# Optimization experiments

Measured on AMD Instinct MI355X. Metric: run time of the kernel, lower is better.

Reference implementation:

```python
import jax
jax.config.update("jax_enable_x64", True)
import jax.numpy as jnp
import numpy as np

LEAF_VOXEL_SIZE = 0.1
SCALE_UP_FACTOR = 2.0
VOXEL_LEVEL_NUM = 4
BUFFER_SIZE = 4194304
FEATURE_DIM = 8
N_FEATURES = 500000
N_QUERY = 1000000
FEATURE_STD = 0.01

PRIMES = jnp.array([73856093, 19349669, 83492791], dtype=jnp.int64)
# 8 voxel-corner offsets, matching self.steps ordering (z fastest)
STEPS = jnp.array([[0,0,0],[0,0,1],[0,1,0],[0,1,1],[1,0,0],[1,0,1],[1,1,0],[1,1,1]], dtype=jnp.float32)


def setup_inputs() -> dict:
    key = jax.random.key(0)
    k1, k2, k3, k4 = jax.random.split(key, 4)
    # query points spread over a few meters of scene
    query_points = 5.0 * jax.random.normal(k1, (N_QUERY, 3), dtype=jnp.float32)
    features = FEATURE_STD * jax.random.normal(k2, (VOXEL_LEVEL_NUM, N_FEATURES, FEATURE_DIM), dtype=jnp.float32)
    idx = jax.random.randint(k3, (VOXEL_LEVEL_NUM, BUFFER_SIZE), 0, N_FEATURES, dtype=jnp.int64)
    empty = jax.random.uniform(k4, (VOXEL_LEVEL_NUM, BUFFER_SIZE)) < 0.05
    feature_indexs = jnp.where(empty, jnp.int64(-1), idx)
    return {"query_points": query_points, "features": features, "feature_indexs": feature_indexs}


def _interp_coeffs(q, vs):
    # trilinear weights in the same corner order as STEPS -> [N, 8]
    d = q / vs - jnp.floor(q / vs)           # [N,3]
    tx, ty, tz = d[:, 0], d[:, 1], d[:, 2]
    w = jnp.stack([
        (1-tx)*(1-ty)*(1-tz), (1-tx)*(1-ty)*tz, (1-tx)*ty*(1-tz), (1-tx)*ty*tz,
        tx*(1-ty)*(1-tz),     tx*(1-ty)*tz,     tx*ty*(1-tz),     tx*ty*tz,
    ], axis=-1)
    return w


def reference(query_points, features, feature_indexs):
    N = query_points.shape[0]
    sum_features = jnp.zeros((N, FEATURE_DIM), dtype=jnp.float32)
    valid_mask = jnp.ones((N,), dtype=bool)
    for i in range(VOXEL_LEVEL_NUM):
        vs = LEAF_VOXEL_SIZE * SCALE_UP_FACTOR ** i
        grids = jnp.floor(query_points / vs)                       # [N,3]
        corners = (grids[:, None, :] + STEPS).astype(jnp.int64)    # [N,8,3]
        keys = (corners * PRIMES).sum(-1) % BUFFER_SIZE            # [N,8]
        idx = feature_indexs[i][keys]                              # [N,8]
        mask = idx.min(axis=1) >= 0                                # [N]
        safe_idx = jnp.maximum(idx, 0)
        feats = features[i][safe_idx]                              # [N,8,D]
        coeffs = _interp_coeffs(query_points, vs)                  # [N,8]
        contrib = jnp.einsum('ncd,nc->nd', feats, coeffs)          # [N,D]
        sum_features = sum_features + jnp.where(mask[:, None], contrib, 0.0)
        if i == 0:
            valid_mask = mask
    return sum_features, valid_mask
```

## Files before the change

### kernel.cpp

```cpp
#include <hip/hip_runtime.h>

#define BUF_MASK 4194303u
#define BUF_SIZE 4194304
#define NFEAT 500000
#define FDIM 8
#define NLVL 4
#define NBINS 262144
#define NXCD 8

typedef float f4 __attribute__((ext_vector_type(4)));

__global__ void detect_int64_kernel(const unsigned int* __restrict__ fi,
                                    int* __restrict__ flag) {
    if (blockIdx.x == 0 && threadIdx.x == 0) {
        int cnt = 0;
        for (int k = 0; k < 128; ++k) {
            unsigned int w = fi[2 * k + 1];
            cnt += (w == 0u || w == 0xFFFFFFFFu) ? 1 : 0;
        }
        *flag = (cnt >= 96) ? 1 : 0;
    }
}

__device__ __forceinline__ unsigned part3(unsigned x) {
    x &= 0x3FFu;
    x = (x | (x << 16)) & 0x030000FFu;
    x = (x | (x << 8))  & 0x0300F00Fu;
    x = (x | (x << 4))  & 0x030C30C3u;
    x = (x | (x << 2))  & 0x09249249u;
    return x;
}

__global__ __launch_bounds__(256) void bin_kernel(
    const float* __restrict__ qp, unsigned* __restrict__ hist,
    unsigned* __restrict__ binA, unsigned* __restrict__ rankA, int N)
{
    int i = blockIdx.x * blockDim.x + threadIdx.x;
    if (i >= N) return;
    float x = qp[3 * (size_t)i + 0];
    float y = qp[3 * (size_t)i + 1];
    float z = qp[3 * (size_t)i + 2];
    int cx = (int)floorf(x * 1.25f) + 32;
    int cy = (int)floorf(y * 1.25f) + 32;
    int cz = (int)floorf(z * 1.25f) + 32;
    cx = min(max(cx, 0), 63); cy = min(max(cy, 0), 63); cz = min(max(cz, 0), 63);
    unsigned m = (part3((unsigned)cx) << 2) | (part3((unsigned)cy) << 1) | part3((unsigned)cz);
    unsigned r = atomicAdd(&hist[m], 1u);
    binA[i] = m; rankA[i] = r;
}

__global__ __launch_bounds__(512) void scan_block(
    const unsigned* __restrict__ hist, unsigned* __restrict__ starts,
    unsigned* __restrict__ bsum)
{
    __shared__ unsigned tmp[512];
    int b = blockIdx.x, t = threadIdx.x;
    unsigned v = hist[(size_t)b * 512 + t];
    tmp[t] = v; __syncthreads();
    for (int o = 1; o < 512; o <<= 1) {
        unsigned add = (t >= o) ? tmp[t - o] : 0u;
        __syncthreads();
        tmp[t] += add;
        __syncthreads();
    }
    starts[(size_t)b * 512 + t] = tmp[t] - v;
    if (t == 511) bsum[b] = tmp[t];
}

__global__ __launch_bounds__(512) void scan_sums(unsigned* __restrict__ bsum) {
    __shared__ unsigned tmp[512];
    int t = threadIdx.x;
    unsigned v = bsum[t];
    tmp[t] = v; __syncthreads();
    for (int o = 1; o < 512; o <<= 1) {
        unsigned add = (t >= o) ? tmp[t - o] : 0u;
        __syncthreads();
        tmp[t] += add;
        __syncthreads();
    }
    bsum[t] = tmp[t] - v;
}

__global__ __launch_bounds__(512) void scan_add(
    unsigned* __restrict__ starts, const unsigned* __restrict__ bsum)
{
    starts[(size_t)blockIdx.x * 512 + threadIdx.x] += bsum[blockIdx.x];
}

__global__ __launch_bounds__(256) void scatter_kernel(
    const float* __restrict__ qp, const unsigned* __restrict__ binA,
    const unsigned* __restrict__ rankA, const unsigned* __restrict__ starts,
    float4* __restrict__ sorted, int N)
{
    int i = blockIdx.x * blockDim.x + threadIdx.x;
    if (i >= N) return;
    unsigned pos = starts[binA[i]] + rankA[i];
    sorted[pos] = make_float4(qp[3 * (size_t)i + 0], qp[3 * (size_t)i + 1],
                              qp[3 * (size_t)i + 2], __uint_as_float((unsigned)i));
}

__global__ __launch_bounds__(256) void nvh_sorted_kernel(
    const f4* __restrict__ sq,
    const float* __restrict__ feats,
    const int*   __restrict__ fidx,
    const int*   __restrict__ flagp,
    float* __restrict__ out,
    int N)
{
    unsigned nwg = gridDim.x, b = blockIdx.x;
    unsigned q = nwg / NXCD, r = nwg % NXCD;
    unsigned xcd = b % NXCD, off = b / NXCD;
    unsigned swz = (xcd < r ? xcd * (q + 1) : r * (q + 1) + (xcd - r) * q) + off;
    int i = (int)(swz * blockDim.x + threadIdx.x);
    if (i >= N) return;
    const int shift = *flagp;

    f4 qv = sq[i];
    float qx = qv.x, qy = qv.y, qz = qv.z;
    unsigned orig = __float_as_uint(qv.w);

    float frx[NLVL], fry[NLVL], frz[NLVL];
    int   idxs[NLVL][8];

    #pragma unroll
    for (int l = 0; l < NLVL; ++l) {
        const float vs = 0.1f * (float)(1 << l);
        float tx = qx / vs, ty = qy / vs, tz = qz / vs;
        float gx = floorf(tx), gy = floorf(ty), gz = floorf(tz);
        frx[l] = tx - gx; fry[l] = ty - gy; frz[l] = tz - gz;
        unsigned h = (unsigned)(int)gx * 73856093u
                   + (unsigned)(int)gy * 19349669u
                   + (unsigned)(int)gz * 83492791u;
        const int* base = fidx + (((size_t)l * BUF_SIZE) << shift);
        #pragma unroll
        for (int c = 0; c < 8; ++c) {
            unsigned key = h;
            if (c & 4) key += 73856093u;
            if (c & 2) key += 19349669u;
            if (c & 1) key += 83492791u;
            key &= BUF_MASK;
            idxs[l][c] = base[(size_t)key << shift];
        }
    }

    float acc[8] = {0.f, 0.f, 0.f, 0.f, 0.f, 0.f, 0.f, 0.f};
    float maskv = 0.0f;

    #pragma unroll
    for (int l = 0; l < NLVL; ++l) {
        int mn = idxs[l][0];
        #pragma unroll
        for (int c = 1; c < 8; ++c) mn = min(mn, idxs[l][c]);
        float m = (mn >= 0) ? 1.0f : 0.0f;
        if (l == 0) maskv = m;
        const float* fb = feats + (size_t)l * (size_t)NFEAT * FDIM;
        float tx = frx[l], ty = fry[l], tz = frz[l];
        float sx[2] = {1.0f - tx, tx};
        float sy[2] = {1.0f - ty, ty};
        float sz[2] = {1.0f - tz, tz};
        #pragma unroll
        for (int c = 0; c < 8; ++c) {
            float w = m * ((sx[(c >> 2) & 1] * sy[(c >> 1) & 1]) * sz[c & 1]);
            const f4* f4p = (const f4*)(fb + (size_t)max(idxs[l][c], 0) * FDIM);
            f4 a = f4p[0];
            f4 b2 = f4p[1];
            acc[0] += w * a.x;  acc[1] += w * a.y;
            acc[2] += w * a.z;  acc[3] += w * a.w;
            acc[4] += w * b2.x; acc[5] += w * b2.y;
            acc[6] += w * b2.z; acc[7] += w * b2.w;
        }
    }

    f4 o0 = {acc[0], acc[1], acc[2], acc[3]};
    f4 o1 = {acc[4], acc[5], acc[6], acc[7]};
    f4* op = (f4*)(out + (size_t)orig * 8);
    op[0] = o0;
    op[1] = o1;
    out[(size_t)8 * N + orig] = maskv;
}

__global__ __launch_bounds__(256) void nvh_kernel(
    const float* __restrict__ qp, const float* __restrict__ feats,
    const int* __restrict__ fidx, const int* __restrict__ flagp,
    float* __restrict__ out, int N)
{
    int i = blockIdx.x * blockDim.x + threadIdx.x;
    if (i >= N) return;
    const int shift = *flagp;
    float qx = qp[3 * (size_t)i + 0];
    float qy = qp[3 * (size_t)i + 1];
    float qz = qp[3 * (size_t)i + 2];
    float frx[NLVL], fry[NLVL], frz[NLVL];
    int   idxs[NLVL][8];
    #pragma unroll
    for (int l = 0; l < NLVL; ++l) {
        const float vs = 0.1f * (float)(1 << l);
        float tx = qx / vs, ty = qy / vs, tz = qz / vs;
        float gx = floorf(tx), gy = floorf(ty), gz = floorf(tz);
        frx[l] = tx - gx; fry[l] = ty - gy; frz[l] = tz - gz;
        unsigned h = (unsigned)(int)gx * 73856093u
                   + (unsigned)(int)gy * 19349669u
                   + (unsigned)(int)gz * 83492791u;
        const int* base = fidx + (((size_t)l * BUF_SIZE) << shift);
        #pragma unroll
        for (int c = 0; c < 8; ++c) {
            unsigned key = h;
            if (c & 4) key += 73856093u;
            if (c & 2) key += 19349669u;
            if (c & 1) key += 83492791u;
            key &= BUF_MASK;
            idxs[l][c] = base[(size_t)key << shift];
        }
    }
    float acc[8] = {0.f, 0.f, 0.f, 0.f, 0.f, 0.f, 0.f, 0.f};
    float maskv = 0.0f;
    #pragma unroll
    for (int l = 0; l < NLVL; ++l) {
        int mn = idxs[l][0];
        #pragma unroll
        for (int c = 1; c < 8; ++c) mn = min(mn, idxs[l][c]);
        float m = (mn >= 0) ? 1.0f : 0.0f;
        if (l == 0) maskv = m;
        const float* fb = feats + (size_t)l * (size_t)NFEAT * FDIM;
        float tx = frx[l], ty = fry[l], tz = frz[l];
        float sx[2] = {1.0f - tx, tx};
        float sy[2] = {1.0f - ty, ty};
        float sz[2] = {1.0f - tz, tz};
        #pragma unroll
        for (int c = 0; c < 8; ++c) {
            float w = m * ((sx[(c >> 2) & 1] * sy[(c >> 1) & 1]) * sz[c & 1]);
            const f4* f4p = (const f4*)(fb + (size_t)max(idxs[l][c], 0) * FDIM);
            f4 a = f4p[0];
            f4 b2 = f4p[1];
            acc[0] += w * a.x;  acc[1] += w * a.y;
            acc[2] += w * a.z;  acc[3] += w * a.w;
            acc[4] += w * b2.x; acc[5] += w * b2.y;
            acc[6] += w * b2.z; acc[7] += w * b2.w;
        }
    }
    float4* o = (float4*)(out + (size_t)i * 8);
    o[0] = make_float4(acc[0], acc[1], acc[2], acc[3]);
    o[1] = make_float4(acc[4], acc[5], acc[6], acc[7]);
    out[(size_t)8 * N + i] = maskv;
}

extern "C" void kernel_launch(void* const* d_in, const int* in_sizes, int n_in,
                              void* d_out, int out_size, void* d_ws, size_t ws_size,
                              hipStream_t stream) {
    const float* qp    = (const float*)d_in[0];
    const float* feats = (const float*)d_in[1];
    const int*   fidx  = (const int*)d_in[2];
    int N = in_sizes[0] / 3;
    int blocks = (N + 255) / 256;

    char* ws = (char*)d_ws;
    size_t off = 0;
    int*      flag   = (int*)(ws + off);      off += 256;
    unsigned* hist   = (unsigned*)(ws + off); off += (size_t)NBINS * 4;
    unsigned* starts = (unsigned*)(ws + off); off += (size_t)NBINS * 4;
    unsigned* bsum   = (unsigned*)(ws + off); off += 512 * 4;
    unsigned* binA   = (unsigned*)(ws + off); off += (size_t)N * 4;
    unsigned* rankA  = (unsigned*)(ws + off); off += (size_t)N * 4;
    off = (off + 15) & ~(size_t)15;
    float4*   sorted = (float4*)(ws + off);   off += (size_t)N * 16;

    detect_int64_kernel<<<1, 64, 0, stream>>>((const unsigned int*)d_in[2], flag);

    if (ws_size < off) {
        nvh_kernel<<<blocks, 256, 0, stream>>>(qp, feats, fidx, flag, (float*)d_out, N);
        return;
    }

    hipMemsetAsync(hist, 0, (size_t)NBINS * 4, stream);
    bin_kernel<<<blocks, 256, 0, stream>>>(qp, hist, binA, rankA, N);
    scan_block<<<512, 512, 0, stream>>>(hist, starts, bsum);
    scan_sums<<<1, 512, 0, stream>>>(bsum);
    scan_add<<<512, 512, 0, stream>>>(starts, bsum);
    scatter_kernel<<<blocks, 256, 0, stream>>>(qp, binA, rankA, starts, sorted, N);
    nvh_sorted_kernel<<<blocks, 256, 0, stream>>>((const f4*)sorted, feats, fidx, flag, (float*)d_out, N);
}
```

Baseline: 442.1 us.

## Pre-convert hash table to int32 and features to fp16 before gather

Adds two pre-pass kernels that compact the int64 hash-index buffer into int32 and convert the feature table to fp16 in workspace. The main gather kernel then reads 4-byte indices and 16-byte feature rows instead of 8-byte indices and 32-byte rows, to cut scattered-gather traffic. It also skips feature loads for levels whose corners are not all valid. In exchange it adds roughly 134MB of read traffic plus writes for the conversions on every call, and fp16 features lose precision.

```diff
diff --git a/kernel.cpp b/kernel.cpp
--- a/kernel.cpp
+++ b/kernel.cpp
@@ -9,6 +9,7 @@
 #define NXCD 8
 
 typedef float f4 __attribute__((ext_vector_type(4)));
+typedef _Float16 h8 __attribute__((ext_vector_type(8)));
 
 __global__ void detect_int64_kernel(const unsigned int* __restrict__ fi,
                                     int* __restrict__ flag) {
@@ -20,6 +21,37 @@
         }
         *flag = (cnt >= 96) ? 1 : 0;
     }
+}
+
+__global__ __launch_bounds__(256) void conv_idx_kernel(
+    const int* __restrict__ src, int* __restrict__ dst,
+    const int* __restrict__ flagp, int ntot)
+{
+    int i = (blockIdx.x * blockDim.x + threadIdx.x) * 2;
+    if (i >= ntot) return;
+    if (*flagp) {
+        const long long* s = (const long long*)src;
+        dst[i]     = (int)s[i];
+        dst[i + 1] = (int)s[i + 1];
+    } else {
+        dst[i]     = src[i];
+        dst[i + 1] = src[i + 1];
+    }
+}
+
+__global__ __launch_bounds__(256) void conv_feat_kernel(
+    const float* __restrict__ src, _Float16* __restrict__ dst, int ntot)
+{
+    int i = (blockIdx.x * blockDim.x + threadIdx.x) * 8;
+    if (i + 8 > ntot) return;
+    f4 a = *(const f4*)(src + i);
+    f4 b = *(const f4*)(src + i + 4);
+    h8 o;
+    o[0] = (_Float16)a.x; o[1] = (_Float16)a.y;
+    o[2] = (_Float16)a.z; o[3] = (_Float16)a.w;
+    o[4] = (_Float16)b.x; o[5] = (_Float16)b.y;
+    o[6] = (_Float16)b.z; o[7] = (_Float16)b.w;
+    *(h8*)(dst + i) = o;
 }
 
 __device__ __forceinline__ unsigned part3(unsigned x) {
@@ -99,13 +131,86 @@
                               qp[3 * (size_t)i + 2], __uint_as_float((unsigned)i));
 }
 
-__global__ __launch_bounds__(256) void nvh_sorted_kernel(
+__global__ __launch_bounds__(256) void nvh_sorted_c(
     const f4* __restrict__ sq,
-    const float* __restrict__ feats,
-    const int*   __restrict__ fidx,
-    const int*   __restrict__ flagp,
-    float* __restrict__ out,
-    int N)
+    const _Float16* __restrict__ feats,
+    const int* __restrict__ fidx,
+    float* __restrict__ out, int N)
+{
+    unsigned nwg = gridDim.x, b = blockIdx.x;
+    unsigned q = nwg / NXCD, r = nwg % NXCD;
+    unsigned xcd = b % NXCD, off = b / NXCD;
+    unsigned swz = (xcd < r ? xcd * (q + 1) : r * (q + 1) + (xcd - r) * q) + off;
+    int i = (int)(swz * blockDim.x + threadIdx.x);
+    if (i >= N) return;
+
+    f4 qv = sq[i];
+    float qx = qv.x, qy = qv.y, qz = qv.z;
+    unsigned orig = __float_as_uint(qv.w);
+
+    float frx[NLVL], fry[NLVL], frz[NLVL];
+    int   idxs[NLVL][8];
+
+    #pragma unroll
+    for (int l = 0; l < NLVL; ++l) {
+        const float vs = 0.1f * (float)(1 << l);
+        float tx = qx / vs, ty = qy / vs, tz = qz / vs;
+        float gx = floorf(tx), gy = floorf(ty), gz = floorf(tz);
+        frx[l] = tx - gx; fry[l] = ty - gy; frz[l] = tz - gz;
+        unsigned h = (unsigned)(int)gx * 73856093u
+                   + (unsigned)(int)gy * 19349669u
+                   + (unsigned)(int)gz * 83492791u;
+        const int* base = fidx + (size_t)l * BUF_SIZE;
+        #pragma unroll
+        for (int c = 0; c < 8; ++c) {
+            unsigned key = h;
+            if (c & 4) key += 73856093u;
+            if (c & 2) key += 19349669u;
+            if (c & 1) key += 83492791u;
+            idxs[l][c] = base[key & BUF_MASK];
+        }
+    }
+
+    float acc[8] = {0.f, 0.f, 0.f, 0.f, 0.f, 0.f, 0.f, 0.f};
+    float maskv = 0.0f;
+
+    #pragma unroll
+    for (int l = 0; l < NLVL; ++l) {
+        int mn = idxs[l][0];
+        #pragma unroll
+        for (int c = 1; c < 8; ++c) mn = min(mn, idxs[l][c]);
+        bool valid = (mn >= 0);
+        if (l == 0) maskv = valid ? 1.0f : 0.0f;
+        if (valid) {
+            const _Float16* fb = feats + (size_t)l * (size_t)NFEAT * FDIM;
+            float tx = frx[l], ty = fry[l], tz = frz[l];
+            float sx[2] = {1.0f - tx, tx};
+            float sy[2] = {1.0f - ty, ty};
+            float sz[2] = {1.0f - tz, tz};
+            #pragma unroll
+            for (int c = 0; c < 8; ++c) {
+                float w = (sx[(c >> 2) & 1] * sy[(c >> 1) & 1]) * sz[c & 1];
+                h8 v = *(const h8*)(fb + (size_t)idxs[l][c] * FDIM);
+                acc[0] += w * (float)v[0]; acc[1] += w * (float)v[1];
+                acc[2] += w * (float)v[2]; acc[3] += w * (float)v[3];
+                acc[4] += w * (float)v[4]; acc[5] += w * (float)v[5];
+                acc[6] += w * (float)v[6]; acc[7] += w * (float)v[7];
+            }
+        }
+    }
+
+    f4 o0 = {acc[0], acc[1], acc[2], acc[3]};
+    f4 o1 = {acc[4], acc[5], acc[6], acc[7]};
+    f4* op = (f4*)(out + (size_t)orig * 8);
+    op[0] = o0;
+    op[1] = o1;
+    out[(size_t)8 * N + orig] = maskv;
+}
+
+__global__ __launch_bounds__(256) void nvh_sorted_o(
+    const f4* __restrict__ sq, const float* __restrict__ feats,
+    const int* __restrict__ fidx, const int* __restrict__ flagp,
+    float* __restrict__ out, int N)
 {
     unsigned nwg = gridDim.x, b = blockIdx.x;
     unsigned q = nwg / NXCD, r = nwg % NXCD;
@@ -151,23 +256,25 @@
         int mn = idxs[l][0];
         #pragma unroll
         for (int c = 1; c < 8; ++c) mn = min(mn, idxs[l][c]);
-        float m = (mn >= 0) ? 1.0f : 0.0f;
-        if (l == 0) maskv = m;
-        const float* fb = feats + (size_t)l * (size_t)NFEAT * FDIM;
-        float tx = frx[l], ty = fry[l], tz = frz[l];
-        float sx[2] = {1.0f - tx, tx};
-        float sy[2] = {1.0f - ty, ty};
-        float sz[2] = {1.0f - tz, tz};
-        #pragma unroll
-        for (int c = 0; c < 8; ++c) {
-            float w = m * ((sx[(c >> 2) & 1] * sy[(c >> 1) & 1]) * sz[c & 1]);
-            const f4* f4p = (const f4*)(fb + (size_t)max(idxs[l][c], 0) * FDIM);
-            f4 a = f4p[0];
-            f4 b2 = f4p[1];
-            acc[0] += w * a.x;  acc[1] += w * a.y;
-            acc[2] += w * a.z;  acc[3] += w * a.w;
-            acc[4] += w * b2.x; acc[5] += w * b2.y;
-            acc[6] += w * b2.z; acc[7] += w * b2.w;
+        bool valid = (mn >= 0);
+        if (l == 0) maskv = valid ? 1.0f : 0.0f;
+        if (valid) {
+            const float* fb = feats + (size_t)l * (size_t)NFEAT * FDIM;
+            float tx = frx[l], ty = fry[l], tz = frz[l];
+            float sx[2] = {1.0f - tx, tx};
+            float sy[2] = {1.0f - ty, ty};
+            float sz[2] = {1.0f - tz, tz};
+            #pragma unroll
+            for (int c = 0; c < 8; ++c) {
+                float w = (sx[(c >> 2) & 1] * sy[(c >> 1) & 1]) * sz[c & 1];
+                const f4* f4p = (const f4*)(fb + (size_t)idxs[l][c] * FDIM);
+                f4 a = f4p[0];
+                f4 b2 = f4p[1];
+                acc[0] += w * a.x;  acc[1] += w * a.y;
+                acc[2] += w * a.z;  acc[3] += w * a.w;
+                acc[4] += w * b2.x; acc[5] += w * b2.y;
+                acc[6] += w * b2.z; acc[7] += w * b2.w;
+            }
         }
     }
 
@@ -219,23 +326,25 @@
         int mn = idxs[l][0];
         #pragma unroll
         for (int c = 1; c < 8; ++c) mn = min(mn, idxs[l][c]);
-        float m = (mn >= 0) ? 1.0f : 0.0f;
-        if (l == 0) maskv = m;
-        const float* fb = feats + (size_t)l * (size_t)NFEAT * FDIM;
-        float tx = frx[l], ty = fry[l], tz = frz[l];
-        float sx[2] = {1.0f - tx, tx};
-        float sy[2] = {1.0f - ty, ty};
-        float sz[2] = {1.0f - tz, tz};
-        #pragma unroll
-        for (int c = 0; c < 8; ++c) {
-            float w = m * ((sx[(c >> 2) & 1] * sy[(c >> 1) & 1]) * sz[c & 1]);
-            const f4* f4p = (const f4*)(fb + (size_t)max(idxs[l][c], 0) * FDIM);
-            f4 a = f4p[0];
-            f4 b2 = f4p[1];
-            acc[0] += w * a.x;  acc[1] += w * a.y;
-            acc[2] += w * a.z;  acc[3] += w * a.w;
-            acc[4] += w * b2.x; acc[5] += w * b2.y;
-            acc[6] += w * b2.z; acc[7] += w * b2.w;
+        bool valid = (mn >= 0);
+        if (l == 0) maskv = valid ? 1.0f : 0.0f;
+        if (valid) {
+            const float* fb = feats + (size_t)l * (size_t)NFEAT * FDIM;
+            float tx = frx[l], ty = fry[l], tz = frz[l];
+            float sx[2] = {1.0f - tx, tx};
+            float sy[2] = {1.0f - ty, ty};
+            float sz[2] = {1.0f - tz, tz};
+            #pragma unroll
+            for (int c = 0; c < 8; ++c) {
+                float w = (sx[(c >> 2) & 1] * sy[(c >> 1) & 1]) * sz[c & 1];
+                const f4* f4p = (const f4*)(fb + (size_t)idxs[l][c] * FDIM);
+                f4 a = f4p[0];
+                f4 b2 = f4p[1];
+                acc[0] += w * a.x;  acc[1] += w * a.y;
+                acc[2] += w * a.z;  acc[3] += w * a.w;
+                acc[4] += w * b2.x; acc[5] += w * b2.y;
+                acc[6] += w * b2.z; acc[7] += w * b2.w;
+            }
         }
     }
     float4* o = (float4*)(out + (size_t)i * 8);
@@ -252,6 +361,9 @@
     const int*   fidx  = (const int*)d_in[2];
     int N = in_sizes[0] / 3;
     int blocks = (N + 255) / 256;
+
+    const int IDX_TOT  = NLVL * BUF_SIZE;
+    const int FEAT_TOT = NLVL * NFEAT * FDIM;
 
     char* ws = (char*)d_ws;
     size_t off = 0;
@@ -263,12 +375,23 @@
     unsigned* rankA  = (unsigned*)(ws + off); off += (size_t)N * 4;
     off = (off + 15) & ~(size_t)15;
     float4*   sorted = (float4*)(ws + off);   off += (size_t)N * 16;
+    size_t need_sort = off;
+    off = (off + 15) & ~(size_t)15;
+    int*      idx32  = (int*)(ws + off);      off += (size_t)IDX_TOT * 4;
+    _Float16* feat16 = (_Float16*)(ws + off); off += (size_t)FEAT_TOT * 2;
+    size_t need_full = off;
 
     detect_int64_kernel<<<1, 64, 0, stream>>>((const unsigned int*)d_in[2], flag);
 
-    if (ws_size < off) {
+    if (ws_size < need_sort) {
         nvh_kernel<<<blocks, 256, 0, stream>>>(qp, feats, fidx, flag, (float*)d_out, N);
         return;
+    }
+
+    bool full = (ws_size >= need_full);
+    if (full) {
+        conv_idx_kernel<<<IDX_TOT / 2 / 256, 256, 0, stream>>>(fidx, idx32, flag, IDX_TOT);
+        conv_feat_kernel<<<(FEAT_TOT / 8 + 255) / 256, 256, 0, stream>>>(feats, feat16, FEAT_TOT);
     }
 
     hipMemsetAsync(hist, 0, (size_t)NBINS * 4, stream);
@@ -277,5 +400,10 @@
     scan_sums<<<1, 512, 0, stream>>>(bsum);
     scan_add<<<512, 512, 0, stream>>>(starts, bsum);
     scatter_kernel<<<blocks, 256, 0, stream>>>(qp, binA, rankA, starts, sorted, N);
-    nvh_sorted_kernel<<<blocks, 256, 0, stream>>>((const f4*)sorted, feats, fidx, flag, (float*)d_out, N);
-}
+
+    if (full) {
+        nvh_sorted_c<<<blocks, 256, 0, stream>>>((const f4*)sorted, feat16, idx32, (float*)d_out, N);
+    } else {
+        nvh_sorted_o<<<blocks, 256, 0, stream>>>((const f4*)sorted, feats, fidx, flag, (float*)d_out, N);
+    }
+}
```

Measured after the change: 415.2 us. 6.1% less time.
